# Optimization experiments

Measured on AMD Instinct MI355X. Metric: run time of the kernel, lower is better.

Reference implementation:

```python
import jax, jax.numpy as jnp
import numpy as np

BATCH = 16
IN_F = 8192
OUT_F = 8192
BITS = 8


def setup_inputs() -> dict:
    key = jax.random.key(0)
    k_x, k_w, k_s, k_b = jax.random.split(key, 4)
    x = jax.random.normal(k_x, (BATCH, IN_F), dtype=jnp.float32)
    # quantized weights: rounded integer values stored as float, in [0, 2**bits - 1]
    qw = jax.random.randint(k_w, (OUT_F, IN_F), 0, 2 ** BITS).astype(jnp.float32)
    # symmetric quantization: scalar scale, zero_point = 0
    scale = jax.random.uniform(k_s, (1,), dtype=jnp.float32, minval=0.005, maxval=0.02)
    zero_point = jnp.zeros((1,), dtype=jnp.float32)
    bias = jax.random.normal(k_b, (OUT_F,), dtype=jnp.float32)
    return {"x": x, "qw": qw, "scale": scale, "zero_point": zero_point, "bias": bias}


def reference(x, qw, scale, zero_point, bias):
    # dequantize: W = (qw - zp) * scale  -> [out_f, in_f]
    w = (qw - zero_point) * scale
    # F.linear: y = x @ W.T + b
    return jnp.matmul(x, w.T) + bias
```

## Files before the change

### kernel.cpp

```cpp
#include <hip/hip_runtime.h>
#include <hip/hip_bf16.h>


constexpr int IN_F  = 8192;
constexpr int OUT_F = 8192;
constexpr int BATCH = 16;
constexpr int KSPLIT = 8;
constexpr int SEG    = IN_F / KSPLIT;
constexpr int ITERS  = SEG / 32;
constexpr int NT     = OUT_F / 16;
constexpr int WPB    = 4;

typedef __attribute__((ext_vector_type(8))) short bf16x8;
typedef __attribute__((ext_vector_type(4))) float f32x4;

__device__ inline short f2bf(float f) {
    __hip_bfloat16 h = __float2bfloat16(f);
    return __builtin_bit_cast(short, h);
}

__global__ __launch_bounds__(256)
void prep_kernel(const float* __restrict__ x, unsigned short* __restrict__ xbf,
                 float* __restrict__ sumxp) {
    __shared__ float red[4];
    const int b = blockIdx.x >> 2;
    const int g = blockIdx.x & 3;
    const int base = b * IN_F + g * (IN_F / 4);
    const int t = threadIdx.x;

    float s = 0.0f;
#pragma unroll
    for (int u = 0; u < 2; ++u) {
        const int i = base + u * 1024 + t * 4;
        const float4 v = *reinterpret_cast<const float4*>(x + i);
        s += v.x + v.y + v.z + v.w;
        ushort4 o;
        o.x = (unsigned short)f2bf(v.x);
        o.y = (unsigned short)f2bf(v.y);
        o.z = (unsigned short)f2bf(v.z);
        o.w = (unsigned short)f2bf(v.w);
        *reinterpret_cast<ushort4*>(xbf + i) = o;
    }
#pragma unroll
    for (int d = 32; d >= 1; d >>= 1) s += __shfl_xor(s, d, 64);
    if ((t & 63) == 0) red[t >> 6] = s;
    __syncthreads();
    if (t == 0) sumxp[blockIdx.x] = red[0] + red[1] + red[2] + red[3];
}

__global__ __launch_bounds__(WPB * 64)
void qlinear_mfma(const unsigned short* __restrict__ xbf,
                  const float* __restrict__ qw,
                  float* __restrict__ part)
{
    __shared__ short a_lds[ITERS * 512];

    const int lane = threadIdx.x & 63;
    const int wave = threadIdx.x >> 6;
    const int wg   = blockIdx.x * WPB + wave;
    const int seg  = wg / NT;
    const int tile = wg - seg * NT;
    const int n0   = tile * 16;
    const int lm   = lane & 15;
    const int lkg  = lane >> 4;
    const int lk   = lkg * 8;

    {
        const unsigned short* srcbase = xbf + lm * IN_F + seg * SEG + lk;
#pragma unroll
        for (int s = 0; s < 8; ++s) {
            const int it = wave * 8 + s;
            const bf16x8 v = *reinterpret_cast<const bf16x8*>(srcbase + it * 32);
            *reinterpret_cast<bf16x8*>(&a_lds[it * 512 + lane * 8]) = v;
        }
    }
    __syncthreads();

    const float* qp = qw + (size_t)(n0 + lm) * IN_F + seg * SEG + lk;

    f32x4 acc = {0.0f, 0.0f, 0.0f, 0.0f};

#pragma unroll 4
    for (int it = 0; it < ITERS; ++it) {
        const bf16x8 a = *reinterpret_cast<const bf16x8*>(&a_lds[it * 512 + lane * 8]);
        const float4 q0 = *reinterpret_cast<const float4*>(qp + it * 32);
        const float4 q1 = *reinterpret_cast<const float4*>(qp + it * 32 + 4);
        bf16x8 bq;
        bq[0] = f2bf(q0.x); bq[1] = f2bf(q0.y);
        bq[2] = f2bf(q0.z); bq[3] = f2bf(q0.w);
        bq[4] = f2bf(q1.x); bq[5] = f2bf(q1.y);
        bq[6] = f2bf(q1.z); bq[7] = f2bf(q1.w);
        acc = __builtin_amdgcn_mfma_f32_16x16x32_bf16(a, bq, acc, 0, 0, 0);
    }

    const int m0 = lkg * 4;
    float* pp = part + ((size_t)seg * BATCH + m0) * OUT_F + n0 + lm;
#pragma unroll
    for (int j = 0; j < 4; ++j)
        pp[(size_t)j * OUT_F] = acc[j];
}

__global__ __launch_bounds__(256)
void qlinear_stage2(const float* __restrict__ part,
                    const float* __restrict__ sumxp,
                    const float* __restrict__ scale_p,
                    const float* __restrict__ zp_p,
                    const float* __restrict__ bias,
                    float* __restrict__ y)
{
    const int i = (blockIdx.x * 256 + threadIdx.x) * 4;
    const int b = i >> 13;
    const float s  = scale_p[0];
    const float sumx = sumxp[b * 4] + sumxp[b * 4 + 1]
                     + sumxp[b * 4 + 2] + sumxp[b * 4 + 3];
    const float zc = zp_p[0] * sumx;
    float4 sum = {0.0f, 0.0f, 0.0f, 0.0f};
#pragma unroll
    for (int seg = 0; seg < KSPLIT; ++seg) {
        const float4 p = *reinterpret_cast<const float4*>(
            part + (size_t)seg * BATCH * OUT_F + i);
        sum.x += p.x; sum.y += p.y; sum.z += p.z; sum.w += p.w;
    }
    const float4 bv = *reinterpret_cast<const float4*>(bias + (i & (OUT_F - 1)));
    float4 out;
    out.x = s * (sum.x - zc) + bv.x;
    out.y = s * (sum.y - zc) + bv.y;
    out.z = s * (sum.z - zc) + bv.z;
    out.w = s * (sum.w - zc) + bv.w;
    *reinterpret_cast<float4*>(y + i) = out;
}

extern "C" void kernel_launch(void* const* d_in, const int* in_sizes, int n_in,
                              void* d_out, int out_size, void* d_ws, size_t ws_size,
                              hipStream_t stream) {
    const float* x     = (const float*)d_in[0];
    const float* qw    = (const float*)d_in[1];
    const float* scale = (const float*)d_in[2];
    const float* zp    = (const float*)d_in[3];
    const float* bias  = (const float*)d_in[4];
    float* y = (float*)d_out;

    float* part = (float*)d_ws;
    unsigned short* xbf = (unsigned short*)(part + (size_t)KSPLIT * BATCH * OUT_F);
    float* sumxp = (float*)(xbf + (size_t)BATCH * IN_F);

    prep_kernel<<<64, 256, 0, stream>>>(x, xbf, sumxp);
    qlinear_mfma<<<KSPLIT * NT / WPB, WPB * 64, 0, stream>>>(xbf, qw, part);
    const int n_elem_blocks = (BATCH * OUT_F / 4) / 256;
    qlinear_stage2<<<n_elem_blocks, 256, 0, stream>>>(part, sumxp, scale, zp, bias, y);
}
```

Measured before the change: 57.41 us.

## Stage weight tiles through swizzled LDS with coalesced row loads

The weight matrix is now loaded cooperatively: each wave reads full contiguous 1 KB rows of qw with float4 per lane, converts them to bf16 and writes them into an XOR-swizzled LDS buffer. MFMA B fragments are then read from LDS. The activation operand is read straight from global memory (L2-resident) instead of being staged in LDS. This replaces the earlier strided per-lane 32-byte weight reads with fully coalesced row reads. In exchange it adds two block barriers per 256-element chunk and serializes the load and compute phases without double buffering.

```diff
diff --git a/kernel.cpp b/kernel.cpp
--- a/kernel.cpp
+++ b/kernel.cpp
@@ -7,16 +7,18 @@
 constexpr int BATCH = 16;
 constexpr int KSPLIT = 8;
 constexpr int SEG    = IN_F / KSPLIT;
-constexpr int ITERS  = SEG / 32;
+constexpr int CHUNK  = 256;
+constexpr int NCHUNK = SEG / CHUNK;
+constexpr int IPC    = CHUNK / 32;
 constexpr int NT     = OUT_F / 16;
 constexpr int WPB    = 4;
 
 typedef __attribute__((ext_vector_type(8))) short bf16x8;
 typedef __attribute__((ext_vector_type(4))) float f32x4;
 
-__device__ inline short f2bf(float f) {
+__device__ inline unsigned short f2bf(float f) {
     __hip_bfloat16 h = __float2bfloat16(f);
-    return __builtin_bit_cast(short, h);
+    return (unsigned short)__builtin_bit_cast(short, h);
 }
 
 __global__ __launch_bounds__(256)
@@ -35,10 +37,10 @@
         const float4 v = *reinterpret_cast<const float4*>(x + i);
         s += v.x + v.y + v.z + v.w;
         ushort4 o;
-        o.x = (unsigned short)f2bf(v.x);
-        o.y = (unsigned short)f2bf(v.y);
-        o.z = (unsigned short)f2bf(v.z);
-        o.w = (unsigned short)f2bf(v.w);
+        o.x = f2bf(v.x);
+        o.y = f2bf(v.y);
+        o.z = f2bf(v.z);
+        o.w = f2bf(v.w);
         *reinterpret_cast<ushort4*>(xbf + i) = o;
     }
 #pragma unroll
@@ -53,48 +55,54 @@
                   const float* __restrict__ qw,
                   float* __restrict__ part)
 {
-    __shared__ short a_lds[ITERS * 512];
+    __shared__ unsigned short blds[64 * CHUNK];
 
     const int lane = threadIdx.x & 63;
     const int wave = threadIdx.x >> 6;
-    const int wg   = blockIdx.x * WPB + wave;
-    const int seg  = wg / NT;
-    const int tile = wg - seg * NT;
-    const int n0   = tile * 16;
+    const int wg0  = blockIdx.x * WPB;
+    const int seg  = wg0 / NT;
+    const int n0b  = (wg0 - seg * NT) * 16;
     const int lm   = lane & 15;
     const int lkg  = lane >> 4;
-    const int lk   = lkg * 8;
+    const int kbase = seg * SEG;
 
-    {
-        const unsigned short* srcbase = xbf + lm * IN_F + seg * SEG + lk;
-#pragma unroll
-        for (int s = 0; s < 8; ++s) {
-            const int it = wave * 8 + s;
-            const bf16x8 v = *reinterpret_cast<const bf16x8*>(srcbase + it * 32);
-            *reinterpret_cast<bf16x8*>(&a_lds[it * 512 + lane * 8]) = v;
-        }
-    }
-    __syncthreads();
+    const unsigned short* xp = xbf + lm * IN_F + kbase + lkg * 8;
 
-    const float* qp = qw + (size_t)(n0 + lm) * IN_F + seg * SEG + lk;
+    const int lrow  = wave * 16 + lm;
+    const int fsw   = (lrow & 7) << 4;
+    const int rbase = lrow * 512 + lkg * 16;
 
     f32x4 acc = {0.0f, 0.0f, 0.0f, 0.0f};
 
-#pragma unroll 4
-    for (int it = 0; it < ITERS; ++it) {
-        const bf16x8 a = *reinterpret_cast<const bf16x8*>(&a_lds[it * 512 + lane * 8]);
-        const float4 q0 = *reinterpret_cast<const float4*>(qp + it * 32);
-        const float4 q1 = *reinterpret_cast<const float4*>(qp + it * 32 + 4);
-        bf16x8 bq;
-        bq[0] = f2bf(q0.x); bq[1] = f2bf(q0.y);
-        bq[2] = f2bf(q0.z); bq[3] = f2bf(q0.w);
-        bq[4] = f2bf(q1.x); bq[5] = f2bf(q1.y);
-        bq[6] = f2bf(q1.z); bq[7] = f2bf(q1.w);
-        acc = __builtin_amdgcn_mfma_f32_16x16x32_bf16(a, bq, acc, 0, 0, 0);
+    for (int c = 0; c < NCHUNK; ++c) {
+        __syncthreads();
+#pragma unroll
+        for (int j = 0; j < 16; ++j) {
+            const int lr = wave * 16 + j;
+            const float4 v = *reinterpret_cast<const float4*>(
+                qw + (size_t)(n0b + lr) * IN_F + kbase + c * CHUNK + lane * 4);
+            ushort4 o;
+            o.x = f2bf(v.x);
+            o.y = f2bf(v.y);
+            o.z = f2bf(v.z);
+            o.w = f2bf(v.w);
+            *reinterpret_cast<ushort4*>(
+                reinterpret_cast<char*>(blds) +
+                lr * 512 + ((lane * 8) ^ ((lr & 7) << 4))) = o;
+        }
+        __syncthreads();
+#pragma unroll
+        for (int it = 0; it < IPC; ++it) {
+            const bf16x8 a = *reinterpret_cast<const bf16x8*>(
+                xp + c * CHUNK + it * 32);
+            const bf16x8 b = *reinterpret_cast<const bf16x8*>(
+                reinterpret_cast<char*>(blds) + ((rbase + it * 64) ^ fsw));
+            acc = __builtin_amdgcn_mfma_f32_16x16x32_bf16(a, b, acc, 0, 0, 0);
+        }
     }
 
     const int m0 = lkg * 4;
-    float* pp = part + ((size_t)seg * BATCH + m0) * OUT_F + n0 + lm;
+    float* pp = part + ((size_t)seg * BATCH + m0) * OUT_F + n0b + wave * 16 + lm;
 #pragma unroll
     for (int j = 0; j < 4; ++j)
         pp[(size_t)j * OUT_F] = acc[j];
```

Measured after the change: 56.20 us (median of 2 runs). -2.1%, faster.
